# Performance work log

Measured on AMD Instinct MI355X. Metric: run time of the kernel, lower is better.

## Reference

```python
import jax, jax.numpy as jnp
import numpy as np

D_MODEL = 1024
NUM_HEADS = 16
HEAD_DIMS = D_MODEL // NUM_HEADS


def setup_inputs() -> dict:
    key = jax.random.key(0)
    k1, k2, k3, k4, k5 = jax.random.split(key, 5)
    B, S = 2, 2048
    x = jax.random.normal(k1, (B, S, D_MODEL), dtype=jnp.float32)
    mask = jnp.zeros((B, S, S), dtype=jnp.float32)  # additive float mask
    # torch Linear weights; stored as (in, out) so y = x @ W + b
    s_in = 1.0 / np.sqrt(D_MODEL)
    Wqkv = jax.random.uniform(k2, (D_MODEL, 3 * D_MODEL), jnp.float32, -s_in, s_in)
    bqkv = jax.random.uniform(k3, (3 * D_MODEL,), jnp.float32, -s_in, s_in)
    Wo = jax.random.uniform(k4, (D_MODEL, D_MODEL), jnp.float32, -s_in, s_in)
    bo = jax.random.uniform(k5, (D_MODEL,), jnp.float32, -s_in, s_in)
    return {"x": x, "mask": mask, "Wqkv": Wqkv, "bqkv": bqkv, "Wo": Wo, "bo": bo}


def reference(x, mask, Wqkv, bqkv, Wo, bo):
    B, S, _ = x.shape
    qkv = x @ Wqkv + bqkv                                   # [B, S, 3*D]
    qkv = qkv.reshape(B, S, NUM_HEADS, 3 * HEAD_DIMS)
    qkv = jnp.transpose(qkv, (0, 2, 1, 3))                  # [B, H, S, 3*hd]
    q, k, v = jnp.split(qkv, 3, axis=-1)                    # each [B, H, S, hd]
    scale = 1.0 / np.sqrt(HEAD_DIMS).astype(np.float32)
    scores = jnp.einsum("bhqd,bhkd->bhqk", q, k) * scale    # [B, H, S, S]
    scores = scores + mask[:, None, :, :]
    attn = jax.nn.softmax(scores, axis=-1)
    values = jnp.einsum("bhqk,bhkd->bhqd", attn, v)         # [B, H, S, hd]
    # Faithful to original: direct row-major reshape (B,H,S,hd)->(B,S,H*hd),
    # WITHOUT transposing heads back (replicates the source's reshape).
    values = values.reshape(B, S, NUM_HEADS * HEAD_DIMS)
    out = values @ Wo + bo
    return out
```

## Files before the change

kernel.cpp:

```cpp
#include <hip/hip_runtime.h>
#include <stdint.h>


#define LOG2E 1.44269504088896340736f

typedef __attribute__((ext_vector_type(4))) float f32x4;
typedef __attribute__((ext_vector_type(8))) short short8v;
typedef __attribute__((ext_vector_type(8))) __bf16 bf16x8;
typedef __attribute__((ext_vector_type(2))) __bf16 bf16x2;
typedef __attribute__((ext_vector_type(4))) unsigned uint4v;

__device__ __forceinline__ unsigned short f2bf(float f) {
  unsigned u = __builtin_bit_cast(unsigned, f);
  u += 0x7FFFu + ((u >> 16) & 1u);
  return (unsigned short)(u >> 16);
}

__device__ __forceinline__ unsigned pack2(float lo, float hi) {
  return (unsigned)f2bf(lo) | ((unsigned)f2bf(hi) << 16);
}

__device__ __forceinline__ unsigned packbf(float lo, float hi) {
  bf16x2 t;
  t[0] = (__bf16)lo;
  t[1] = (__bf16)hi;
  return __builtin_bit_cast(unsigned, t);
}

__device__ __forceinline__ f32x4 mfma16(short8v a, short8v b, f32x4 c) {
  return __builtin_amdgcn_mfma_f32_16x16x32_bf16(
      __builtin_bit_cast(bf16x8, a), __builtin_bit_cast(bf16x8, b), c, 0, 0, 0);
}

__device__ __forceinline__ void gload_lds16(const void* g, void* l) {
  __builtin_amdgcn_global_load_lds(
      (const __attribute__((address_space(1))) void*)(uintptr_t)g,
      (__attribute__((address_space(3))) void*)(uintptr_t)l, 16, 0, 0);
}

__global__ void cvt_x_kernel(const float4* __restrict__ src,
                             uint2* __restrict__ dst, int n4) {
  int i = blockIdx.x * 256 + threadIdx.x;
  if (i < n4) {
    float4 v = src[i];
    dst[i] = make_uint2(pack2(v.x, v.y), pack2(v.z, v.w));
  }
}

__global__ void transpose_cvt_kernel(const float* __restrict__ src,
                                     unsigned short* __restrict__ dst,
                                     int R, int C) {
  __shared__ unsigned short tile[64][65];
  int tc = threadIdx.x & 63;
  int tr = threadIdx.x >> 6;
  int c0 = blockIdx.x * 64;
  int r0 = blockIdx.y * 64;
#pragma unroll
  for (int i = 0; i < 16; ++i) {
    int r = tr * 16 + i;
    tile[r][tc] = f2bf(src[(size_t)(r0 + r) * C + c0 + tc]);
  }
  __syncthreads();
#pragma unroll
  for (int i = 0; i < 16; ++i) {
    int cc = tr * 16 + i;
    dst[(size_t)(c0 + cc) * R + r0 + tc] = tile[tc][cc];
  }
}

__global__ __launch_bounds__(256, 2)
void gemm_qkv_kernel(const unsigned short* __restrict__ xbf,
                     const unsigned short* __restrict__ WT,
                     const float* __restrict__ bias,
                     unsigned short* __restrict__ Qb,
                     unsigned short* __restrict__ Kb,
                     unsigned short* __restrict__ VbT) {
  const int K = 1024;
  __shared__ __align__(16) unsigned short As[128 * 64];
  __shared__ __align__(16) unsigned short Bs[128 * 64];
  int tid = threadIdx.x;
  int lane = tid & 63;
  int wid = tid >> 6;
  int m0 = blockIdx.y * 128;
  int n0 = blockIdx.x * 128;
  int wm = (wid >> 1) * 64;
  int wn = (wid & 1) * 64;
  f32x4 acc[4][4] = {};
  for (int k0 = 0; k0 < K; k0 += 64) {
#pragma unroll
    for (int it = 0; it < 4; ++it) {
      int G = it * 256 + tid;
      int r = G >> 3, g = G & 7;
      int sg = g ^ (r & 7);
      gload_lds16(xbf + (size_t)(m0 + r) * K + k0 + sg * 8, &As[G * 8]);
      gload_lds16(WT + (size_t)(n0 + r) * K + k0 + sg * 8, &Bs[G * 8]);
    }
    __syncthreads();
#pragma unroll
    for (int ks = 0; ks < 2; ++ks) {
      short8v a[4], bf[4];
      int kg = ks * 4 + (lane >> 4);
#pragma unroll
      for (int i = 0; i < 4; ++i) {
        int ra = wm + i * 16 + (lane & 15);
        a[i] = *(const short8v*)&As[ra * 64 + ((kg ^ (ra & 7)) << 3)];
        int rb = wn + i * 16 + (lane & 15);
        bf[i] = *(const short8v*)&Bs[rb * 64 + ((kg ^ (rb & 7)) << 3)];
      }
#pragma unroll
      for (int i = 0; i < 4; ++i)
#pragma unroll
        for (int j = 0; j < 4; ++j)
          acc[i][j] = mfma16(a[i], bf[j], acc[i][j]);
    }
    __syncthreads();
  }
#pragma unroll
  for (int i = 0; i < 4; ++i) {
#pragma unroll
    for (int j = 0; j < 4; ++j) {
      int n = n0 + wn + j * 16 + (lane & 15);
      float bv = bias[n];
      int h = n / 192;
      int rr = n - h * 192;
      int t = rr >> 6;
      int d = rr & 63;
#pragma unroll
      for (int rg = 0; rg < 4; ++rg) {
        int m = m0 + wm + i * 16 + ((lane >> 4) << 2) + rg;
        int b = m >> 11, s = m & 2047;
        unsigned short val = f2bf(acc[i][j][rg] + bv);
        int bh = b * 16 + h;
        if (t == 2) {
          VbT[((size_t)bh * 64 + d) * 2048 + s] = val;
        } else {
          unsigned short* dst = (t == 0) ? Qb : Kb;
          dst[((size_t)bh * 2048 + s) * 64 + d] = val;
        }
      }
    }
  }
}


#define ATTN_STAGE(kt_, bi_)                                                  \
  do {                                                                        \
    _Pragma("unroll") for (int it_ = 0; it_ < 2; ++it_) {                     \
      int G_ = it_ * 256 + tid;                                               \
      int r_ = G_ >> 3, g_ = G_ & 7;                                          \
      int sg_ = g_ ^ (r_ & 7);                                                \
      gload_lds16(Kb + bh_off + (size_t)((kt_)*64 + r_) * 64 + sg_ * 8,       \
                  &Ks[bi_][G_ * 8]);                                          \
      gload_lds16(VbT + bh_off + (size_t)r_ * 2048 + (kt_)*64 + sg_ * 8,      \
                  &Vs[bi_][G_ * 8]);                                          \
    }                                                                         \
  } while (0)

#define ATTN_TILE(kt_, CUR_)                                                  \
  do {                                                                        \
    if ((kt_) < 31) ATTN_STAGE((kt_) + 1, (CUR_) ^ 1);                        \
                \
    f32x4 mk_[4];                                                             \
    _Pragma("unroll") for (int f = 0; f < 4; ++f)                             \
        mk_[f] = *(const f32x4*)(mrowq + (size_t)(kt_)*64 + f * 16);          \
                            \
    f32x4 sf[4] = {};                                                         \
    _Pragma("unroll") for (int ks = 0; ks < 2; ++ks) {                        \
      short8v qa = ks ? qa1 : qa0;                                            \
      int kg = ks * 4 + hi;                                                   \
      _Pragma("unroll") for (int f = 0; f < 4; ++f) {                         \
        int row = f * 16 + lq;                                                \
        short8v kb =                                                          \
            *(const short8v*)&Ks[CUR_][row * 64 + ((kg ^ (row & 7)) << 3)];   \
        sf[f] = mfma16(kb, qa, sf[f]);                                        \
      }                                                                       \
    }                                                                         \
    _Pragma("unroll") for (int f = 0; f < 4; ++f)                             \
        _Pragma("unroll") for (int r = 0; r < 4; ++r)                         \
            sf[f][r] = fmaf(sf[f][r], 0.125f, mk_[f][r]);                     \
                 \
    float mx0_ = fmaxf(fmaxf(sf[0][0], sf[0][1]), fmaxf(sf[0][2], sf[0][3])); \
    float mx1_ = fmaxf(fmaxf(sf[1][0], sf[1][1]), fmaxf(sf[1][2], sf[1][3])); \
    float mx2_ = fmaxf(fmaxf(sf[2][0], sf[2][1]), fmaxf(sf[2][2], sf[2][3])); \
    float mx3_ = fmaxf(fmaxf(sf[3][0], sf[3][1]), fmaxf(sf[3][2], sf[3][3])); \
    float mt_ = fmaxf(fmaxf(mx0_, mx1_), fmaxf(mx2_, mx3_));                  \
    mt_ = fmaxf(mt_, __shfl_xor(mt_, 16));                                    \
    mt_ = fmaxf(mt_, __shfl_xor(mt_, 32));                                    \
                                                               \
    if (!__all(mt_ <= m_s + THR)) {                                           \
      float mn_ = fmaxf(m_s, mt_);                                            \
      float al_ = exp2f((m_s - mn_) * LOG2E);                                 \
      m_s = mn_;                                                              \
      mLs = mn_ * LOG2E;                                                      \
      l_s *= al_;                                                             \
      float a0_ = __shfl(al_, (lane & 48) | hi4);                             \
      float a1_ = __shfl(al_, (lane & 48) | (hi4 + 1));                       \
      float a2_ = __shfl(al_, (lane & 48) | (hi4 + 2));                       \
      float a3_ = __shfl(al_, (lane & 48) | (hi4 + 3));                       \
      _Pragma("unroll") for (int f = 0; f < 4; ++f) {                         \
        o[f][0] *= a0_; o[f][1] *= a1_; o[f][2] *= a2_; o[f][3] *= a3_;       \
      }                                                                       \
    }                                                                         \
            \
    unsigned pk_[4][2];                                                       \
    _Pragma("unroll") for (int f = 0; f < 4; ++f) {                           \
      float p0_ = exp2f(fmaf(sf[f][0], LOG2E, -mLs));                         \
      float p1_ = exp2f(fmaf(sf[f][1], LOG2E, -mLs));                         \
      float p2_ = exp2f(fmaf(sf[f][2], LOG2E, -mLs));                         \
      float p3_ = exp2f(fmaf(sf[f][3], LOG2E, -mLs));                         \
      l_s += (p0_ + p1_) + (p2_ + p3_);                                       \
      pk_[f][0] = packbf(p0_, p1_);                                           \
      pk_[f][1] = packbf(p2_, p3_);                                           \
    }                                                                         \
     \
     \
     \
     \
    _Pragma("unroll") for (int ks = 0; ks < 2; ++ks) {                        \
      unsigned s0_ = __shfl(pk_[2 * ks][0], sha_);                            \
      unsigned s1_ = __shfl(pk_[2 * ks][1], sha_);                            \
      unsigned s2_ = __shfl(pk_[2 * ks][0], shb_);                            \
      unsigned s3_ = __shfl(pk_[2 * ks][1], shb_);                            \
      unsigned t0_ = __shfl(pk_[2 * ks + 1][0], sha_);                        \
      unsigned t1_ = __shfl(pk_[2 * ks + 1][1], sha_);                        \
      unsigned t2_ = __shfl(pk_[2 * ks + 1][0], shb_);                        \
      unsigned t3_ = __shfl(pk_[2 * ks + 1][1], shb_);                        \
      uint4v au_;                                                             \
      au_[0] = hilo_ ? s0_ : t0_;                                             \
      au_[1] = hilo_ ? s1_ : t1_;                                             \
      au_[2] = hilo_ ? s2_ : t2_;                                             \
      au_[3] = hilo_ ? s3_ : t3_;                                             \
      short8v pa = __builtin_bit_cast(short8v, au_);                          \
      int kg = ks * 4 + hi;                                                   \
      _Pragma("unroll") for (int f = 0; f < 4; ++f) {                         \
        int vrow_ = f * 16 + lq;                                              \
        short8v vb_ =                                                         \
            *(const short8v*)&Vs[CUR_][vrow_ * 64 + ((kg ^ (vrow_ & 7)) << 3)]; \
        o[f] = mfma16(pa, vb_, o[f]);                                         \
      }                                                                       \
    }                                                                         \
    __syncthreads();                                                          \
  } while (0)

__global__ __launch_bounds__(256, 4)
void attn_kernel(const unsigned short* __restrict__ Qb,
                 const unsigned short* __restrict__ Kb,
                 const unsigned short* __restrict__ VbT,
                 const float* __restrict__ mask,
                 unsigned short* __restrict__ vals) {
  __shared__ __align__(16) unsigned short Ks[2][64 * 64];
  __shared__ __align__(16) unsigned short Vs[2][64 * 64];
  int tid = threadIdx.x;
  int lane = tid & 63;
  int wid = tid >> 6;
  int lq = lane & 15;
  int hi = lane >> 4;
  int hi4 = hi << 2;
  int sha_ = lq | ((hi & 1) << 5);
  int shb_ = sha_ | 16;
  bool hilo_ = (hi < 2);
  int h = blockIdx.x & 15;
  int qt = (blockIdx.x >> 4) & 31;
  int b = blockIdx.x >> 9;
  int bh = b * 16 + h;
  size_t bh_off = (size_t)bh * 2048 * 64;
  int q0 = qt * 64 + wid * 16;

  const unsigned short* qptr =
      Qb + bh_off + (size_t)(q0 + lq) * 64 + (hi << 3);
  short8v qa0 = *(const short8v*)qptr;
  short8v qa1 = *(const short8v*)(qptr + 32);

  f32x4 o[4] = {};
  float m_s = -1e30f, l_s = 0.f, mLs = 0.f;

  const float* mrowq = mask + ((size_t)b * 2048 + q0 + lq) * 2048 + hi4;

  const float THR = 4.0f;

  ATTN_STAGE(0, 0);
  __syncthreads();

  for (int t = 0; t < 16; ++t) {
    ATTN_TILE(2 * t, 0);
    ATTN_TILE(2 * t + 1, 1);
  }

  l_s += __shfl_xor(l_s, 16);
  l_s += __shfl_xor(l_s, 32);
  float ri_ = 1.0f / l_s;
  float rv_[4];
#pragma unroll
  for (int r = 0; r < 4; ++r) rv_[r] = __shfl(ri_, (lane & 48) | (hi4 + r));

#pragma unroll
  for (int f = 0; f < 4; ++f)
#pragma unroll
    for (int r = 0; r < 4; ++r) {
      int s = q0 + hi4 + r;
      int d = f * 16 + lq;
      int s2 = h * 128 + (s >> 4);
      int c2 = ((s & 15) << 6) + d;
      vals[((size_t)b * 2048 + s2) * 1024 + c2] = f2bf(o[f][r] * rv_[r]);
    }
}


#define OUT_STAGE(k0_, bi_)                                                   \
  do {                                                                        \
    _Pragma("unroll") for (int it_ = 0; it_ < 4; ++it_) {                     \
      int G_ = it_ * 256 + tid;                                               \
      int r_ = G_ >> 3, g_ = G_ & 7;                                          \
      int sg_ = g_ ^ (r_ & 7);                                                \
      gload_lds16(vals + (size_t)(m0 + r_) * 1024 + (k0_) + sg_ * 8,          \
                  &As[bi_][G_ * 8]);                                          \
    }                                                                         \
    _Pragma("unroll") for (int it_ = 0; it_ < 2; ++it_) {                     \
      int G_ = it_ * 256 + tid;                                               \
      int r_ = G_ >> 3, g_ = G_ & 7;                                          \
      int sg_ = g_ ^ (r_ & 7);                                                \
      gload_lds16(WoT + (size_t)(n0 + r_) * 1024 + (k0_) + sg_ * 8,           \
                  &Bs[bi_][G_ * 8]);                                          \
    }                                                                         \
  } while (0)

#define OUT_STEP(k0_, CUR_)                                                   \
  do {                                                                        \
    if ((k0_) + 64 < 1024) OUT_STAGE((k0_) + 64, (CUR_) ^ 1);                 \
    _Pragma("unroll") for (int ks = 0; ks < 2; ++ks) {                        \
      short8v a_[4], b_[2];                                                   \
      int kg = ks * 4 + hi;                                                   \
      _Pragma("unroll") for (int i = 0; i < 4; ++i) {                         \
        int ra = wm + i * 16 + lq;                                            \
        a_[i] = *(const short8v*)&As[CUR_][ra * 64 + ((kg ^ (ra & 7)) << 3)]; \
      }                                                                       \
      _Pragma("unroll") for (int j = 0; j < 2; ++j) {                         \
        int rb = wn + j * 16 + lq;                                            \
        b_[j] = *(const short8v*)&Bs[CUR_][rb * 64 + ((kg ^ (rb & 7)) << 3)]; \
      }                                                                       \
      _Pragma("unroll") for (int i = 0; i < 4; ++i)                           \
          _Pragma("unroll") for (int j = 0; j < 2; ++j)                       \
              acc[i][j] = mfma16(a_[i], b_[j], acc[i][j]);                    \
    }                                                                         \
    __syncthreads();                                                          \
  } while (0)

__global__ __launch_bounds__(256, 2)
void gemm_out_kernel(const unsigned short* __restrict__ vals,
                     const unsigned short* __restrict__ WoT,
                     const float* __restrict__ bo,
                     float* __restrict__ out) {
  __shared__ __align__(16) unsigned short As[2][128 * 64];
  __shared__ __align__(16) unsigned short Bs[2][64 * 64];
  int tid = threadIdx.x;
  int lane = tid & 63;
  int wid = tid >> 6;
  int lq = lane & 15;
  int hi = lane >> 4;
  int m0 = blockIdx.y * 128;
  int n0 = blockIdx.x * 64;
  int wm = (wid >> 1) * 64;
  int wn = (wid & 1) * 32;
  f32x4 acc[4][2] = {};

  OUT_STAGE(0, 0);
  __syncthreads();
#pragma unroll 1
  for (int kk = 0; kk < 8; ++kk) {
    OUT_STEP(kk * 128, 0);
    OUT_STEP(kk * 128 + 64, 1);
  }

#pragma unroll
  for (int i = 0; i < 4; ++i) {
#pragma unroll
    for (int j = 0; j < 2; ++j) {
      int n = n0 + wn + j * 16 + lq;
      float bv = bo[n];
#pragma unroll
      for (int rg = 0; rg < 4; ++rg) {
        int m = m0 + wm + i * 16 + (hi << 2) + rg;
        out[(size_t)m * 1024 + n] = acc[i][j][rg] + bv;
      }
    }
  }
}

extern "C" void kernel_launch(void* const* d_in, const int* in_sizes, int n_in,
                              void* d_out, int out_size, void* d_ws,
                              size_t ws_size, hipStream_t stream) {
  const float* x    = (const float*)d_in[0];
  const float* mask = (const float*)d_in[1];
  const float* Wqkv = (const float*)d_in[2];
  const float* bqkv = (const float*)d_in[3];
  const float* Wo   = (const float*)d_in[4];
  const float* bo   = (const float*)d_in[5];
  float* out = (float*)d_out;

  char* ws = (char*)d_ws;
  unsigned short* xbf   = (unsigned short*)(ws);
  unsigned short* WqkvT = (unsigned short*)(ws + 8388608);
  unsigned short* WoT   = (unsigned short*)(ws + 14680064);
  unsigned short* Qb    = (unsigned short*)(ws + 16777216);
  unsigned short* Kb    = (unsigned short*)(ws + 25165824);
  unsigned short* VbT   = (unsigned short*)(ws + 33554432);
  unsigned short* vals  = xbf;

  hipLaunchKernelGGL(cvt_x_kernel, dim3(4096), dim3(256), 0, stream,
                     (const float4*)x, (uint2*)xbf, 1048576);
  hipLaunchKernelGGL(transpose_cvt_kernel, dim3(48, 16), dim3(256), 0, stream,
                     Wqkv, WqkvT, 1024, 3072);
  hipLaunchKernelGGL(transpose_cvt_kernel, dim3(16, 16), dim3(256), 0, stream,
                     Wo, WoT, 1024, 1024);
  hipLaunchKernelGGL(gemm_qkv_kernel, dim3(24, 32), dim3(256), 0, stream,
                     xbf, WqkvT, bqkv, Qb, Kb, VbT);
  hipLaunchKernelGGL(attn_kernel, dim3(1024), dim3(256), 0, stream,
                     Qb, Kb, VbT, mask, vals);
  hipLaunchKernelGGL(gemm_out_kernel, dim3(16, 32), dim3(256), 0, stream,
                     vals, WoT, bo, out);
}
```

Baseline: 258.1 us.

## Merge prep kernels, prefetch mask one tile ahead, drop P-shuffles via permuted V reads

Folds the x conversion and both weight transpose-converts into one launch, dispatched by block index, which saves two kernel launches. In attention, the additive-mask tile for the next key block is loaded while the current tile computes, using double-buffered registers so its latency is hidden. The cross-lane shuffles that rearranged the softmax probabilities into MFMA A-operand layout are removed. V is instead read from LDS as two 4-element halves in a matching permuted k order, which trades eight shuffles per step for narrower LDS reads and extra registers for the mask buffers.

```diff
diff --git a/kernel.cpp b/kernel.cpp
--- a/kernel.cpp
+++ b/kernel.cpp
@@ -6,6 +6,7 @@
 
 typedef __attribute__((ext_vector_type(4))) float f32x4;
 typedef __attribute__((ext_vector_type(8))) short short8v;
+typedef __attribute__((ext_vector_type(4))) short short4v;
 typedef __attribute__((ext_vector_type(8))) __bf16 bf16x8;
 typedef __attribute__((ext_vector_type(2))) __bf16 bf16x2;
 typedef __attribute__((ext_vector_type(4))) unsigned uint4v;
@@ -38,23 +39,33 @@
       (__attribute__((address_space(3))) void*)(uintptr_t)l, 16, 0, 0);
 }
 
-__global__ void cvt_x_kernel(const float4* __restrict__ src,
-                             uint2* __restrict__ dst, int n4) {
-  int i = blockIdx.x * 256 + threadIdx.x;
-  if (i < n4) {
-    float4 v = src[i];
-    dst[i] = make_uint2(pack2(v.x, v.y), pack2(v.z, v.w));
-  }
-}
-
-__global__ void transpose_cvt_kernel(const float* __restrict__ src,
-                                     unsigned short* __restrict__ dst,
-                                     int R, int C) {
+__global__ void prep_kernel(const float4* __restrict__ x4,
+                            uint2* __restrict__ xd,
+                            const float* __restrict__ Wq,
+                            unsigned short* __restrict__ WqT,
+                            const float* __restrict__ Wo,
+                            unsigned short* __restrict__ WoT) {
   __shared__ unsigned short tile[64][65];
+  int bb = blockIdx.x;
+  if (bb < 4096) {
+    int i = bb * 256 + threadIdx.x;
+    float4 v = x4[i];
+    xd[i] = make_uint2(pack2(v.x, v.y), pack2(v.z, v.w));
+    return;
+  }
+  const float* src;
+  unsigned short* dst;
+  int C, bx, by;
+  if (bb < 4864) {
+    int idx = bb - 4096;
+    src = Wq; dst = WqT; C = 3072; bx = idx % 48; by = idx / 48;
+  } else {
+    int idx = bb - 4864;
+    src = Wo; dst = WoT; C = 1024; bx = idx & 15; by = idx >> 4;
+  }
   int tc = threadIdx.x & 63;
   int tr = threadIdx.x >> 6;
-  int c0 = blockIdx.x * 64;
-  int r0 = blockIdx.y * 64;
+  int c0 = bx * 64, r0 = by * 64;
 #pragma unroll
   for (int i = 0; i < 16; ++i) {
     int r = tr * 16 + i;
@@ -64,7 +75,7 @@
 #pragma unroll
   for (int i = 0; i < 16; ++i) {
     int cc = tr * 16 + i;
-    dst[(size_t)(c0 + cc) * R + r0 + tc] = tile[tc][cc];
+    dst[(size_t)(c0 + cc) * 1024 + r0 + tc] = tile[tc][cc];
   }
 }
 
@@ -156,13 +167,14 @@
     }                                                                         \
   } while (0)
 
-#define ATTN_TILE(kt_, CUR_)                                                  \
+#define ATTN_TILE(kt_, CUR_, MKC_, MKN_)                                      \
   do {                                                                        \
-    if ((kt_) < 31) ATTN_STAGE((kt_) + 1, (CUR_) ^ 1);                        \
-                \
-    f32x4 mk_[4];                                                             \
-    _Pragma("unroll") for (int f = 0; f < 4; ++f)                             \
-        mk_[f] = *(const f32x4*)(mrowq + (size_t)(kt_)*64 + f * 16);          \
+    if ((kt_) < 31) {                                                         \
+      ATTN_STAGE((kt_) + 1, (CUR_) ^ 1);                                      \
+      _Pragma("unroll") for (int f = 0; f < 4; ++f)                           \
+          MKN_[f] =                                                           \
+              *(const f32x4*)(mrowq + (size_t)((kt_) + 1) * 64 + f * 16);     \
+    }                                                                         \
                             \
     f32x4 sf[4] = {};                                                         \
     _Pragma("unroll") for (int ks = 0; ks < 2; ++ks) {                        \
@@ -177,7 +189,7 @@
     }                                                                         \
     _Pragma("unroll") for (int f = 0; f < 4; ++f)                             \
         _Pragma("unroll") for (int r = 0; r < 4; ++r)                         \
-            sf[f][r] = fmaf(sf[f][r], 0.125f, mk_[f][r]);                     \
+            sf[f][r] = fmaf(sf[f][r], 0.125f, MKC_[f][r]);                    \
                  \
     float mx0_ = fmaxf(fmaxf(sf[0][0], sf[0][1]), fmaxf(sf[0][2], sf[0][3])); \
     float mx1_ = fmaxf(fmaxf(sf[1][0], sf[1][1]), fmaxf(sf[1][2], sf[1][3])); \
@@ -212,30 +224,28 @@
       pk_[f][0] = packbf(p0_, p1_);                                           \
       pk_[f][1] = packbf(p2_, p3_);                                           \
     }                                                                         \
-     \
-     \
-     \
-     \
+    \
+    \
     _Pragma("unroll") for (int ks = 0; ks < 2; ++ks) {                        \
-      unsigned s0_ = __shfl(pk_[2 * ks][0], sha_);                            \
-      unsigned s1_ = __shfl(pk_[2 * ks][1], sha_);                            \
-      unsigned s2_ = __shfl(pk_[2 * ks][0], shb_);                            \
-      unsigned s3_ = __shfl(pk_[2 * ks][1], shb_);                            \
-      unsigned t0_ = __shfl(pk_[2 * ks + 1][0], sha_);                        \
-      unsigned t1_ = __shfl(pk_[2 * ks + 1][1], sha_);                        \
-      unsigned t2_ = __shfl(pk_[2 * ks + 1][0], shb_);                        \
-      unsigned t3_ = __shfl(pk_[2 * ks + 1][1], shb_);                        \
       uint4v au_;                                                             \
-      au_[0] = hilo_ ? s0_ : t0_;                                             \
-      au_[1] = hilo_ ? s1_ : t1_;                                             \
-      au_[2] = hilo_ ? s2_ : t2_;                                             \
-      au_[3] = hilo_ ? s3_ : t3_;                                             \
+      au_[0] = pk_[2 * ks][0];                                                \
+      au_[1] = pk_[2 * ks][1];                                                \
+      au_[2] = pk_[2 * ks + 1][0];                                            \
+      au_[3] = pk_[2 * ks + 1][1];                                            \
       short8v pa = __builtin_bit_cast(short8v, au_);                          \
-      int kg = ks * 4 + hi;                                                   \
       _Pragma("unroll") for (int f = 0; f < 4; ++f) {                         \
         int vrow_ = f * 16 + lq;                                              \
-        short8v vb_ =                                                         \
-            *(const short8v*)&Vs[CUR_][vrow_ * 64 + ((kg ^ (vrow_ & 7)) << 3)]; \
+        int blkA_ = 4 * ks + (hi >> 1);                                       \
+        int eA_ = vrow_ * 64 + (((blkA_) ^ (vrow_ & 7)) << 3) +               \
+                  ((hi & 1) << 2);                                            \
+        int eB_ = vrow_ * 64 + (((blkA_ + 2) ^ (vrow_ & 7)) << 3) +           \
+                  ((hi & 1) << 2);                                            \
+        short4v vlo_ = *(const short4v*)&Vs[CUR_][eA_];                       \
+        short4v vhi_ = *(const short4v*)&Vs[CUR_][eB_];                       \
+        short8v vb_;                                                          \
+        vb_[0] = vlo_[0]; vb_[1] = vlo_[1]; vb_[2] = vlo_[2];                 \
+        vb_[3] = vlo_[3]; vb_[4] = vhi_[0]; vb_[5] = vhi_[1];                 \
+        vb_[6] = vhi_[2]; vb_[7] = vhi_[3];                                   \
         o[f] = mfma16(pa, vb_, o[f]);                                         \
       }                                                                       \
     }                                                                         \
@@ -256,9 +266,6 @@
   int lq = lane & 15;
   int hi = lane >> 4;
   int hi4 = hi << 2;
-  int sha_ = lq | ((hi & 1) << 5);
-  int shb_ = sha_ | 16;
-  bool hilo_ = (hi < 2);
   int h = blockIdx.x & 15;
   int qt = (blockIdx.x >> 4) & 31;
   int b = blockIdx.x >> 9;
@@ -278,12 +285,15 @@
 
   const float THR = 4.0f;
 
+  f32x4 mkA[4], mkB[4];
+#pragma unroll
+  for (int f = 0; f < 4; ++f) mkA[f] = *(const f32x4*)(mrowq + f * 16);
   ATTN_STAGE(0, 0);
   __syncthreads();
 
   for (int t = 0; t < 16; ++t) {
-    ATTN_TILE(2 * t, 0);
-    ATTN_TILE(2 * t + 1, 1);
+    ATTN_TILE(2 * t, 0, mkA, mkB);
+    ATTN_TILE(2 * t + 1, 1, mkB, mkA);
   }
 
   l_s += __shfl_xor(l_s, 16);
@@ -406,12 +416,8 @@
   unsigned short* VbT   = (unsigned short*)(ws + 33554432);
   unsigned short* vals  = xbf;
 
-  hipLaunchKernelGGL(cvt_x_kernel, dim3(4096), dim3(256), 0, stream,
-                     (const float4*)x, (uint2*)xbf, 1048576);
-  hipLaunchKernelGGL(transpose_cvt_kernel, dim3(48, 16), dim3(256), 0, stream,
-                     Wqkv, WqkvT, 1024, 3072);
-  hipLaunchKernelGGL(transpose_cvt_kernel, dim3(16, 16), dim3(256), 0, stream,
-                     Wo, WoT, 1024, 1024);
+  hipLaunchKernelGGL(prep_kernel, dim3(5120), dim3(256), 0, stream,
+                     (const float4*)x, (uint2*)xbf, Wqkv, WqkvT, Wo, WoT);
   hipLaunchKernelGGL(gemm_qkv_kernel, dim3(24, 32), dim3(256), 0, stream,
                      xbf, WqkvT, bqkv, Qb, Kb, VbT);
   hipLaunchKernelGGL(attn_kernel, dim3(1024), dim3(256), 0, stream,
```

Result: faster. 244.9 us (-5.1%).
